# Optimization experiments

Measured on AMD Instinct MI355X. Metric: run time of the kernel, lower is better.

## Reference

```python
import jax, jax.numpy as jnp
import numpy as np
from jax import lax

LEAK = 0.2  # LeakyReLU negative slope used both in flow_conv and as act_type


def conv2d(x, w, b):
    # x: (N,Cin,H,W), w: (Cout,Cin,kh,kw) -> 'SAME' padding, stride 1
    out = lax.conv_general_dilated(x, w, (1, 1), 'SAME',
                                   dimension_numbers=('NCHW', 'OIHW', 'NCHW'))
    return out + b[None, :, None, None]


def leaky(x):
    return jnp.where(x >= 0, x, LEAK * x)


def bilinear_sample(im, ix, iy):
    # im: (C,H,W); ix,iy: (H,W) absolute pixel coords; zero padding (grid_sample default)
    C, H, W = im.shape
    x0 = jnp.floor(ix)
    y0 = jnp.floor(iy)

    def gather(xi, yi):
        valid = (xi >= 0) & (xi <= W - 1) & (yi >= 0) & (yi <= H - 1)
        xc = jnp.clip(xi, 0, W - 1).astype(jnp.int32)
        yc = jnp.clip(yi, 0, H - 1).astype(jnp.int32)
        return im[:, yc, xc] * valid[None].astype(im.dtype)

    wx1 = ix - x0
    wy1 = iy - y0
    wx0 = 1.0 - wx1
    wy0 = 1.0 - wy1
    return (gather(x0, y0) * (wx0 * wy0)[None]
            + gather(x0 + 1, y0) * (wx1 * wy0)[None]
            + gather(x0, y0 + 1) * (wx0 * wy1)[None]
            + gather(x0 + 1, y0 + 1) * (wx1 * wy1)[None])


def warp_all(h, flows):
    # h: (B,Ch,H,W); flows: (B,L,2,H,W). Matches warp(prev_h, -flow) with
    # torch F.grid_sample (bilinear, zero padding, align_corners=False).
    B, Ch, H, W = h.shape
    dt = h.dtype
    xx = jnp.arange(W, dtype=dt)
    yy = jnp.arange(H, dtype=dt)
    vx = xx[None, None, None, :] - flows[:, :, 0]  # grid + (-flow), x coord
    vy = yy[None, None, :, None] - flows[:, :, 1]
    xn = 2.0 * vx / max(W - 1, 1) - 1.0  # normalize to [-1,1]
    yn = 2.0 * vy / max(H - 1, 1) - 1.0
    ix = ((xn + 1.0) * W - 1.0) * 0.5  # unnormalize, align_corners=False
    iy = ((yn + 1.0) * H - 1.0) * 0.5
    samp = jax.vmap(jax.vmap(bilinear_sample, in_axes=(None, 0, 0)),
                    in_axes=(0, 0, 0))
    out = samp(h, ix, iy)  # (B,L,Ch,H,W)
    return out.reshape(B, -1, H, W)  # (B, L*Ch, H, W), same order as torch.cat


def setup_inputs() -> dict:
    key = jax.random.key(0)
    ks = jax.random.split(key, 8)
    B, S, C, H, W = 4, 6, 8, 96, 96
    Ch, L = 64, 13
    sc = lambda fan_in: 1.0 / np.sqrt(fan_in)
    return {
        'inputs': jax.random.normal(ks[0], (B, S, C, H, W), jnp.float32),
        'states': jnp.zeros((B, Ch, H, W), jnp.float32),
        'fw1': jax.random.normal(ks[1], (32, C + Ch, 3, 3), jnp.float32) * sc((C + Ch) * 9),
        'fb1': jnp.zeros((32,), jnp.float32),
        'fw2': jax.random.normal(ks[2], (2 * L, 32, 3, 3), jnp.float32) * sc(32 * 9),
        'fb2': jnp.zeros((2 * L,), jnp.float32),
        'i2h_w': jax.random.normal(ks[3], (3 * Ch, C, 3, 3), jnp.float32) * sc(C * 9),
        'i2h_b': jnp.zeros((3 * Ch,), jnp.float32),
        'ret_w': jax.random.normal(ks[4], (3 * Ch, L * Ch, 1, 1), jnp.float32) * sc(L * Ch),
        'ret_b': jnp.zeros((3 * Ch,), jnp.float32),
        'seq_len': 6,
    }


def reference(inputs, states, fw1, fb1, fw2, fb2, i2h_w, i2h_b, ret_w, ret_b, seq_len):
    B, S, C, H, W = inputs.shape
    Ch = states.shape[1]
    # precompute i2h over all timesteps (as in the torch module)
    i2h = conv2d(inputs.reshape(B * S, C, H, W), i2h_w, i2h_b)
    i2h = i2h.reshape(B, S, 3 * Ch, H, W)

    def step(h, xs):
        x_t, i2h_t = xs  # (B,C,H,W), (B,3Ch,H,W)
        f = leaky(conv2d(jnp.concatenate([x_t, h], axis=1), fw1, fb1))
        flows = conv2d(f, fw2, fb2)  # (B, 2L, H, W)
        flows = flows.reshape(B, flows.shape[1] // 2, 2, H, W)
        warped = warp_all(h, flows)  # (B, L*Ch, H, W)
        h2h = conv2d(warped, ret_w, ret_b)  # (B, 3Ch, H, W)
        i1, i2, i3 = jnp.split(i2h_t, 3, axis=1)
        h1, h2, h3 = jnp.split(h2h, 3, axis=1)
        r = jax.nn.sigmoid(i1 + h1)
        u = jax.nn.sigmoid(i2 + h2)
        m = leaky(i3 + r * h3)
        nh = u * h + (1.0 - u) * m
        return nh, nh

    xs = (jnp.moveaxis(inputs, 0, 1), jnp.moveaxis(i2h, 0, 1))  # time-major
    last_h, outs = lax.scan(step, states, xs)
    return jnp.moveaxis(outs, 0, 1), last_h  # ((B,S,Ch,H,W), (B,Ch,H,W))
```

## Files before the change

### kernel.cpp

```cpp
#include <hip/hip_runtime.h>
#include <hip/hip_bf16.h>
#include <math.h>

#define Bn 4
#define Sn 6
#define Cin 8
#define Hh 96
#define Ww 96
#define HW (Hh*Ww)
#define Chn 64
#define Ln 13
#define LCh (Ln*Chn)
#define OC3 (3*Chn)
#define LEAK 0.2f

typedef __hip_bfloat16 bf16;
typedef __attribute__((ext_vector_type(8))) short short8v;
typedef __attribute__((ext_vector_type(4))) short short4v;
typedef __attribute__((ext_vector_type(4))) float f32x4;

__device__ __forceinline__ float b2f(bf16 v){ return __bfloat162float(v); }
__device__ __forceinline__ bf16  f2b(float v){ return __float2bfloat16(v); }
__device__ __forceinline__ unsigned short bbits(bf16 v){ union{bf16 b; unsigned short s;} u; u.b=v; return u.s; }
__device__ __forceinline__ float us2f(unsigned short u){
    union{unsigned int i; float f;} x; x.i = ((unsigned)u)<<16; return x.f;
}
__device__ __forceinline__ const int4* rfl_ptr(const int4* p){
    uintptr_t v = (uintptr_t)p;
    int lo = __builtin_amdgcn_readfirstlane((int)(v & 0xFFFFFFFFu));
    int hi = __builtin_amdgcn_readfirstlane((int)(v >> 32));
    return (const int4*)(((uintptr_t)(unsigned)hi << 32) | (unsigned)lo);
}

__device__ __forceinline__ int4 mk_meta(float fx, float fy, int xc, int y){
    float ix = ((float)xc - fx) * (96.0f/95.0f) - 0.5f;
    float iy = ((float)y  - fy) * (96.0f/95.0f) - 0.5f;
    float x0f = floorf(ix), y0f = floorf(iy);
    float wx1 = ix - x0f,  wy1 = iy - y0f;
    float wx0 = 1.f - wx1, wy0 = 1.f - wy1;
    float vx0 = (x0f >=  0.f && x0f <= 95.f) ? 1.f : 0.f;
    float vx1 = (x0f >= -1.f && x0f <= 94.f) ? 1.f : 0.f;
    float vy0 = (y0f >=  0.f && y0f <= 95.f) ? 1.f : 0.f;
    float vy1 = (y0f >= -1.f && y0f <= 94.f) ? 1.f : 0.f;
    int xi0 = (int)fminf(fmaxf(x0f,      0.f), 95.f);
    int xi1 = (int)fminf(fmaxf(x0f+1.f,  0.f), 95.f);
    int yi0 = (int)fminf(fmaxf(y0f,      0.f), 95.f);
    int yi1 = (int)fminf(fmaxf(y0f+1.f,  0.f), 95.f);
    union { _Float16 h[2]; int i; } pz, pw;
    pz.h[0] = (_Float16)(wx0*wy0*vx0*vy0);
    pz.h[1] = (_Float16)(wx1*wy0*vx1*vy0);
    pw.h[0] = (_Float16)(wx0*wy1*vx0*vy1);
    pw.h[1] = (_Float16)(wx1*wy1*vx1*vy1);
    int4 m;
    m.x = (yi0*Ww+xi0) | ((yi0*Ww+xi1)<<16);
    m.y = (yi1*Ww+xi0) | ((yi1*Ww+xi1)<<16);
    m.z = pz.i; m.w = pw.i;
    return m;
}

__global__ void k_prep(const float* __restrict__ fw1, const float* __restrict__ fw2,
                       const float* __restrict__ wi,  const float* __restrict__ rw,
                       bf16* __restrict__ W1b, bf16* __restrict__ W2b,
                       bf16* __restrict__ Wi,  bf16* __restrict__ Wb)
{
    int i = blockIdx.x*256 + threadIdx.x;
    if (i < 21504){
        int oc = i/672, k = i%672; float v = 0.f;
        if (k < 648){ int tap = k/72, ic = k%72; v = fw1[(size_t)oc*648 + ic*9 + tap]; }
        W1b[i] = f2b(v);
    } else if (i < 30720){
        int j = i-21504; int oc = j/288, k = j%288; float v = 0.f;
        if (oc < 26){ int tap = k/32, ic = k%32; v = fw2[(size_t)oc*288 + ic*9 + tap]; }
        W2b[j] = f2b(v);
    } else if (i < 49152){
        int j = i-30720; int oc = j/96, k = j%96; float v = 0.f;
        if (k < 72){ int tap = k/8, ic = k%8; v = wi[(size_t)oc*72 + ic*9 + tap]; }
        Wi[j] = f2b(v);
    } else if (i < 208896){
        int j = i-49152; Wb[j] = f2b(rw[j]);
    }
}

__global__ void k_packx(const float* __restrict__ x, bf16* __restrict__ x_hwc)
{
    __shared__ unsigned short tx[8][68];
    int bs = blockIdx.y, pix0 = blockIdx.x*64, tid = threadIdx.x;
    #pragma unroll
    for (int it=0; it<2; ++it){
        int idx = it*256 + tid, ic = idx>>6, p = idx&63;
        tx[ic][p] = bbits(f2b(x[((size_t)bs*Cin + ic)*HW + pix0 + p]));
    }
    __syncthreads();
    unsigned short* dst = (unsigned short*)x_hwc;
    #pragma unroll
    for (int it=0; it<2; ++it){
        int j = it*256 + tid, p = j>>3, c = j&7;
        dst[((size_t)bs*HW + pix0 + p)*8 + c] = tx[c][p];
    }
}

__global__ void k_packh0(const float* __restrict__ s, bf16* __restrict__ hwc)
{
    __shared__ unsigned short t[64][65];
    int b = blockIdx.y, pix0 = blockIdx.x*64, tid = threadIdx.x;
    unsigned short* dst = (unsigned short*)hwc;
    #pragma unroll
    for (int it=0; it<16; ++it){
        int idx = it*256 + tid, c = idx>>6, p = idx&63;
        t[c][p] = bbits(f2b(s[((size_t)b*Chn + c)*HW + pix0 + p]));
    }
    __syncthreads();
    #pragma unroll
    for (int it=0; it<16; ++it){
        int idx = it*256 + tid, p = idx>>6, c = idx&63;
        dst[((size_t)b*HW + pix0 + p)*Chn + c] = t[c][p];
    }
}

__global__ __launch_bounds__(384) void k_front(const bf16* __restrict__ x_hwc,
        const bf16* __restrict__ h_hwc,
        const bf16* __restrict__ Wi,  const float* __restrict__ ib,
        const bf16* __restrict__ W1b, const float* __restrict__ fb1,
        bf16* __restrict__ i2h_hwc, bf16* __restrict__ f_hwc, int t)
{
    __shared__ bf16 tile[3*98*72];
    int y = blockIdx.x, b = blockIdx.y, tid = threadIdx.x;
    const bf16* xb = x_hwc + (size_t)(b*Sn + t)*HW*8;
    const bf16* hb = h_hwc + (size_t)b*HW*64;
    for (int s = tid; s < 294; s += 384){
        int r = s/98, px = s%98 - 1, yy = y + r - 1;
        float4* dst = (float4*)&tile[s*72];
        if (yy>=0 && yy<Hh && px>=0 && px<Ww){
            size_t gp = (size_t)yy*Ww + px;
            dst[0] = *(const float4*)(xb + gp*8);
            const float4* hsrc = (const float4*)(hb + gp*64);
            #pragma unroll
            for (int q=0;q<8;++q) dst[1+q] = hsrc[q];
        } else {
            float4 z{0,0,0,0};
            #pragma unroll
            for (int q=0;q<9;++q) dst[q] = z;
        }
    }
    __syncthreads();
    int wv = tid>>6, lane = tid&63, x0 = wv*16, n = lane&15, kg = lane>>4;
    int pix = y*Ww + x0 + n;

    {
        f32x4 acc[12];
        #pragma unroll
        for (int m=0;m<12;++m) acc[m] = f32x4{0,0,0,0};
        #pragma unroll
        for (int kk=0; kk<3; ++kk){
            int g = kk*4 + kg;
            int tap = (g > 8) ? 8 : g;
            int dy = tap/3, dx = tap%3;
            short8v bv = *(const short8v*)&tile[((dy*98) + (x0+n) + dx)*72];
            #pragma unroll
            for (int m=0;m<12;++m){
                short8v av = *(const short8v*)(Wi + (size_t)(m*16 + n)*96 + g*8);
                acc[m] = __builtin_amdgcn_mfma_f32_16x16x32_bf16(av, bv, acc[m], 0,0,0);
            }
        }
        size_t prow = ((size_t)b*HW + pix)*192;
        #pragma unroll
        for (int m=0;m<12;++m){
            short4v sv;
            #pragma unroll
            for (int r=0;r<4;++r){
                int oc = m*16 + kg*4 + r;
                sv[r] = (short)bbits(f2b(acc[m][r] + ib[oc]));
            }
            *(short4v*)&i2h_hwc[prow + m*16 + kg*4] = sv;
        }
    }

    {
        f32x4 acc0{0,0,0,0}, acc1{0,0,0,0};
        #pragma unroll
        for (int kk=0; kk<21; ++kk){
            int g = kk*4 + kg;
            int gc = (g > 80) ? 80 : g;
            int tap = gc/9, ch0 = (gc%9)*8;
            int dy = tap/3, dx = tap%3;
            short8v bv = *(const short8v*)&tile[(((dy*98) + (x0+n) + dx))*72 + ch0];
            short8v a0 = *(const short8v*)(W1b + (size_t)n*672 + g*8);
            short8v a1 = *(const short8v*)(W1b + (size_t)(16+n)*672 + g*8);
            acc0 = __builtin_amdgcn_mfma_f32_16x16x32_bf16(a0, bv, acc0, 0,0,0);
            acc1 = __builtin_amdgcn_mfma_f32_16x16x32_bf16(a1, bv, acc1, 0,0,0);
        }
        size_t prow = (size_t)b*HW + pix;
        #pragma unroll
        for (int mt=0; mt<2; ++mt){
            f32x4 a = mt ? acc1 : acc0;
            short4v sv;
            #pragma unroll
            for (int r=0;r<4;++r){
                int oc = mt*16 + kg*4 + r;
                float v = a[r] + fb1[oc];
                sv[r] = (short)bbits(f2b((v >= 0.f) ? v : LEAK*v));
            }
            *(short4v*)&f_hwc[prow*32 + mt*16 + kg*4] = sv;
        }
    }
}

__global__ __launch_bounds__(384) void k_conv2meta(const bf16* __restrict__ f_hwc,
        const bf16* __restrict__ W2b, const float* __restrict__ fb2,
        int4* __restrict__ meta)
{
    __shared__ bf16 tile[3*98*32];
    int y = blockIdx.x, b = blockIdx.y, tid = threadIdx.x;
    const bf16* fb = f_hwc + (size_t)b*HW*32;
    for (int s = tid; s < 294; s += 384){
        int r = s/98, px = s%98 - 1, yy = y + r - 1;
        float4* dst = (float4*)&tile[s*32];
        if (yy>=0 && yy<Hh && px>=0 && px<Ww){
            const float4* src = (const float4*)(fb + ((size_t)yy*Ww + px)*32);
            #pragma unroll
            for (int q=0;q<4;++q) dst[q] = src[q];
        } else {
            float4 z{0,0,0,0};
            #pragma unroll
            for (int q=0;q<4;++q) dst[q] = z;
        }
    }
    __syncthreads();
    int wv = tid>>6, lane = tid&63, x0 = wv*16, n = lane&15, kg = lane>>4;
    f32x4 acc0{0,0,0,0}, acc1{0,0,0,0};
    #pragma unroll
    for (int kk=0; kk<9; ++kk){
        int g = kk*4 + kg;
        int tap = g>>2, ch0 = (g&3)*8;
        int dy = tap/3, dx = tap%3;
        short8v bv = *(const short8v*)&tile[(((dy*98) + (x0+n) + dx))*32 + ch0];
        short8v a0 = *(const short8v*)(W2b + (size_t)n*288 + g*8);
        short8v a1 = *(const short8v*)(W2b + (size_t)(16+n)*288 + g*8);
        acc0 = __builtin_amdgcn_mfma_f32_16x16x32_bf16(a0, bv, acc0, 0,0,0);
        acc1 = __builtin_amdgcn_mfma_f32_16x16x32_bf16(a1, bv, acc1, 0,0,0);
    }
    int xc = x0 + n, pix = y*Ww + xc;
    int4* mb = meta + (size_t)b*Ln*HW + pix;
    {
        float v0 = acc0[0] + fb2[kg*4+0], v1 = acc0[1] + fb2[kg*4+1];
        float v2 = acc0[2] + fb2[kg*4+2], v3 = acc0[3] + fb2[kg*4+3];
        mb[(size_t)(2*kg  )*HW] = mk_meta(v0, v1, xc, y);
        mb[(size_t)(2*kg+1)*HW] = mk_meta(v2, v3, xc, y);
    }
    if (kg < 3){
        float v0 = acc1[0] + fb2[16+kg*4+0], v1 = acc1[1] + fb2[16+kg*4+1];
        mb[(size_t)(8+2*kg)*HW] = mk_meta(v0, v1, xc, y);
        if (kg < 2){
            float v2 = acc1[2] + fb2[16+kg*4+2], v3 = acc1[3] + fb2[16+kg*4+3];
            mb[(size_t)(9+2*kg)*HW] = mk_meta(v2, v3, xc, y);
        }
    }
}

__global__ __launch_bounds__(256) void k_fused(const int4* __restrict__ meta,
        const bf16* __restrict__ h_cur, const bf16* __restrict__ Wb,
        const float* __restrict__ rb, const bf16* __restrict__ i2h_hwc,
        bf16* __restrict__ h_nxt, float* __restrict__ out, int t)
{
    __shared__ bf16 wlds[32*LCh];
    char* ldsb = (char*)wlds;
    int tid = threadIdx.x, wv = tid>>6, lane = tid&63;
    int b = blockIdx.y, pix0 = blockIdx.x*32;
    const bf16* hb = h_cur + (size_t)b*HW*64;
    const unsigned short* hsu = (const unsigned short*)hb;
    int c = lane;

    const int4* mwp = rfl_ptr(meta + (size_t)b*Ln*HW + pix0 + wv);

    int mzA[8], mwA[8], mzB[8], mwB[8];
    unsigned short gA0[8], gA1[8], gA2[8], gA3[8];
    unsigned short gB0[8], gB1[8], gB2[8], gB3[8];

#define ISSUE(L, MZ, MW, G0, G1, G2, G3)                                \
    {                                                                   \
        _Pragma("unroll")                                               \
        for (int j=0;j<8;++j){                                          \
            int4 m = mwp[(size_t)(L)*HW + 4*j];                         \
            int sx = __builtin_amdgcn_readfirstlane(m.x);               \
            int sy = __builtin_amdgcn_readfirstlane(m.y);               \
            MZ[j] = __builtin_amdgcn_readfirstlane(m.z);                \
            MW[j] = __builtin_amdgcn_readfirstlane(m.w);                \
            G0[j] = hsu[(size_t)(sx & 0xFFFF)*64 + c];                  \
            G1[j] = hsu[(size_t)((unsigned)sx >> 16)*64 + c];           \
            G2[j] = hsu[(size_t)(sy & 0xFFFF)*64 + c];                  \
            G3[j] = hsu[(size_t)((unsigned)sy >> 16)*64 + c];           \
        }                                                               \
    }
#define CONSUME(L, MZ, MW, G0, G1, G2, G3)                              \
    {                                                                   \
        _Pragma("unroll")                                               \
        for (int j=0;j<8;++j){                                          \
            union { int i; _Float16 h[2]; } uz, uw;                     \
            uz.i = MZ[j]; uw.i = MW[j];                                 \
            float v = us2f(G0[j])*(float)uz.h[0]                        \
                    + us2f(G1[j])*(float)uz.h[1]                        \
                    + us2f(G2[j])*(float)uw.h[0]                        \
                    + us2f(G3[j])*(float)uw.h[1];                       \
            int px = wv + 4*j;                                          \
            *(bf16*)(ldsb + px*1664 + ((((L)*64 + c)*2) ^ ((px&7)<<4))) \
                = f2b(v);                                               \
        }                                                               \
    }

    ISSUE(0, mzA, mwA, gA0, gA1, gA2, gA3);
    ISSUE(1, mzB, mwB, gB0, gB1, gB2, gB3);
    CONSUME(0, mzA, mwA, gA0, gA1, gA2, gA3);
    ISSUE(2, mzA, mwA, gA0, gA1, gA2, gA3);
    CONSUME(1, mzB, mwB, gB0, gB1, gB2, gB3);
    ISSUE(3, mzB, mwB, gB0, gB1, gB2, gB3);
    CONSUME(2, mzA, mwA, gA0, gA1, gA2, gA3);
    ISSUE(4, mzA, mwA, gA0, gA1, gA2, gA3);
    CONSUME(3, mzB, mwB, gB0, gB1, gB2, gB3);
    ISSUE(5, mzB, mwB, gB0, gB1, gB2, gB3);
    CONSUME(4, mzA, mwA, gA0, gA1, gA2, gA3);
    ISSUE(6, mzA, mwA, gA0, gA1, gA2, gA3);
    CONSUME(5, mzB, mwB, gB0, gB1, gB2, gB3);
    ISSUE(7, mzB, mwB, gB0, gB1, gB2, gB3);
    CONSUME(6, mzA, mwA, gA0, gA1, gA2, gA3);
    ISSUE(8, mzA, mwA, gA0, gA1, gA2, gA3);
    CONSUME(7, mzB, mwB, gB0, gB1, gB2, gB3);
    ISSUE(9, mzB, mwB, gB0, gB1, gB2, gB3);
    CONSUME(8, mzA, mwA, gA0, gA1, gA2, gA3);
    ISSUE(10, mzA, mwA, gA0, gA1, gA2, gA3);
    CONSUME(9, mzB, mwB, gB0, gB1, gB2, gB3);
    ISSUE(11, mzB, mwB, gB0, gB1, gB2, gB3);
    CONSUME(10, mzA, mwA, gA0, gA1, gA2, gA3);
    ISSUE(12, mzA, mwA, gA0, gA1, gA2, gA3);
    CONSUME(11, mzB, mwB, gB0, gB1, gB2, gB3);
    CONSUME(12, mzA, mwA, gA0, gA1, gA2, gA3);
#undef ISSUE
#undef CONSUME

    int col = lane & 15, kg = lane >> 4;
    int pxa = pix0 + col, pxb = pxa + 16;
    short4v hva = *(const short4v*)&hb[(size_t)pxa*64 + wv*16 + kg*4];
    short4v hvb = *(const short4v*)&hb[(size_t)pxb*64 + wv*16 + kg*4];
    const bf16* ia = i2h_hwc + ((size_t)b*HW + pxa)*192 + wv*16 + kg*4;
    const bf16* ibp= i2h_hwc + ((size_t)b*HW + pxb)*192 + wv*16 + kg*4;
    short4v i1a = *(const short4v*)(ia);
    short4v i2a = *(const short4v*)(ia + 64);
    short4v i3a = *(const short4v*)(ia + 128);
    short4v i1b = *(const short4v*)(ibp);
    short4v i2b = *(const short4v*)(ibp + 64);
    short4v i3b = *(const short4v*)(ibp + 128);
    __syncthreads();

    const short8v* a0 = (const short8v*)(Wb + (size_t)((wv+0)*16+col)*LCh + kg*8);
    const short8v* a1 = (const short8v*)(Wb + (size_t)((wv+4)*16+col)*LCh + kg*8);
    const short8v* a2 = (const short8v*)(Wb + (size_t)((wv+8)*16+col)*LCh + kg*8);
    f32x4 c0a{0,0,0,0}, c1a{0,0,0,0}, c2a{0,0,0,0};
    f32x4 c0b{0,0,0,0}, c1b{0,0,0,0}, c2b{0,0,0,0};
    int swz = (col&7)<<4;
    #pragma unroll 2
    for (int kk=0; kk<26; ++kk){
        short8v av0 = a0[kk*4], av1 = a1[kk*4], av2 = a2[kk*4];
        int offa = col*1664 + ((kk*64 + kg*16) ^ swz);
        int offb = (col+16)*1664 + ((kk*64 + kg*16) ^ swz);
        short8v bva = *(const short8v*)(ldsb + offa);
        short8v bvb = *(const short8v*)(ldsb + offb);
        c0a = __builtin_amdgcn_mfma_f32_16x16x32_bf16(av0, bva, c0a, 0,0,0);
        c0b = __builtin_amdgcn_mfma_f32_16x16x32_bf16(av0, bvb, c0b, 0,0,0);
        c1a = __builtin_amdgcn_mfma_f32_16x16x32_bf16(av1, bva, c1a, 0,0,0);
        c1b = __builtin_amdgcn_mfma_f32_16x16x32_bf16(av1, bvb, c1b, 0,0,0);
        c2a = __builtin_amdgcn_mfma_f32_16x16x32_bf16(av2, bva, c2a, 0,0,0);
        c2b = __builtin_amdgcn_mfma_f32_16x16x32_bf16(av2, bvb, c2b, 0,0,0);
    }

    float nha[4], nhb[4];
    #pragma unroll
    for (int r=0; r<4; ++r){
        int cc = wv*16 + kg*4 + r;
        float h1 = c0a[r] + rb[cc];
        float h2 = c1a[r] + rb[cc+64];
        float h3 = c2a[r] + rb[cc+128];
        float rg = 1.f/(1.f + expf(-(us2f((unsigned short)i1a[r]) + h1)));
        float u  = 1.f/(1.f + expf(-(us2f((unsigned short)i2a[r]) + h2)));
        float mp = us2f((unsigned short)i3a[r]) + rg*h3;
        float m  = (mp >= 0.f) ? mp : LEAK*mp;
        float nh = u*us2f((unsigned short)hva[r]) + (1.f - u)*m;
        nha[r] = nh;
        out[(((size_t)(b*Sn+t))*Chn + cc)*HW + pxa] = nh;
        if (t == Sn-1)
            out[(size_t)Bn*Sn*Chn*HW + ((size_t)b*Chn + cc)*HW + pxa] = nh;
    }
    #pragma unroll
    for (int r=0; r<4; ++r){
        int cc = wv*16 + kg*4 + r;
        float h1 = c0b[r] + rb[cc];
        float h2 = c1b[r] + rb[cc+64];
        float h3 = c2b[r] + rb[cc+128];
        float rg = 1.f/(1.f + expf(-(us2f((unsigned short)i1b[r]) + h1)));
        float u  = 1.f/(1.f + expf(-(us2f((unsigned short)i2b[r]) + h2)));
        float mp = us2f((unsigned short)i3b[r]) + rg*h3;
        float m  = (mp >= 0.f) ? mp : LEAK*mp;
        float nh = u*us2f((unsigned short)hvb[r]) + (1.f - u)*m;
        nhb[r] = nh;
        out[(((size_t)(b*Sn+t))*Chn + cc)*HW + pxb] = nh;
        if (t == Sn-1)
            out[(size_t)Bn*Sn*Chn*HW + ((size_t)b*Chn + cc)*HW + pxb] = nh;
    }
    short4v sva, svb;
    #pragma unroll
    for (int r=0; r<4; ++r){
        sva[r] = (short)bbits(f2b(nha[r]));
        svb[r] = (short)bbits(f2b(nhb[r]));
    }
    *(short4v*)&h_nxt[((size_t)b*HW + pxa)*64 + wv*16 + kg*4] = sva;
    *(short4v*)&h_nxt[((size_t)b*HW + pxb)*64 + wv*16 + kg*4] = svb;
}

extern "C" void kernel_launch(void* const* d_in, const int* in_sizes, int n_in,
                              void* d_out, int out_size, void* d_ws, size_t ws_size,
                              hipStream_t stream) {
    const float* inputs = (const float*)d_in[0];
    const float* states = (const float*)d_in[1];
    const float* fw1    = (const float*)d_in[2];
    const float* fb1    = (const float*)d_in[3];
    const float* fw2    = (const float*)d_in[4];
    const float* fb2    = (const float*)d_in[5];
    const float* i2h_w  = (const float*)d_in[6];
    const float* i2h_b  = (const float*)d_in[7];
    const float* ret_w  = (const float*)d_in[8];
    const float* ret_b  = (const float*)d_in[9];
    float* out = (float*)d_out;

    char* ws = (char*)d_ws;
    bf16* h_hwcA  = (bf16*)(ws);
    bf16* h_hwcB  = (bf16*)(ws +  4718592);
    bf16* x_hwc   = (bf16*)(ws +  9437184);
    bf16* i2h_hwc = (bf16*)(ws + 12976128);
    bf16* f_hwc   = (bf16*)(ws + 27131904);
    int4* meta    = (int4*)(ws + 29491200);
    bf16* W1b     = (bf16*)(ws + 37158912);
    bf16* W2b     = (bf16*)(ws + 37201920);
    bf16* Wi      = (bf16*)(ws + 37220352);
    bf16* Wb      = (bf16*)(ws + 37257216);

    k_prep  <<<dim3(816),        256, 0, stream>>>(fw1, fw2, i2h_w, ret_w,
                                                   W1b, W2b, Wi, Wb);
    k_packx <<<dim3(144, Bn*Sn), 256, 0, stream>>>(inputs, x_hwc);
    k_packh0<<<dim3(144, Bn),    256, 0, stream>>>(states, h_hwcA);

    bf16* h_cur = h_hwcA;
    bf16* h_nxt = h_hwcB;
    for (int t = 0; t < Sn; ++t) {
        k_front    <<<dim3(96, Bn),  384, 0, stream>>>(x_hwc, h_cur, Wi, i2h_b,
                                                       W1b, fb1, i2h_hwc, f_hwc, t);
        k_conv2meta<<<dim3(96, Bn),  384, 0, stream>>>(f_hwc, W2b, fb2, meta);
        k_fused    <<<dim3(288, Bn), 256, 0, stream>>>(meta, h_cur, Wb, ret_b,
                                                       i2h_hwc, h_nxt, out, t);
        bf16* tmp = h_cur; h_cur = h_nxt; h_nxt = tmp;
    }
}
```

Measured before the change: 742.7 us.

## Double k_fused block to 512 threads, halving per-wave gather and MFMA work

k_fused now runs 8 waves per block instead of 4. Each wave gathers 4 pixels per flow instead of 8, and in the GEMM handles one 16-pixel half with three accumulators instead of two halves with six. This cuts per-thread registers and serial work so more waves can hide gather latency. In exchange, each Wb A-fragment is loaded by twice as many waves, and the 53KB LDS per block may limit how many blocks fit on a CU.

```diff
diff --git a/kernel.cpp b/kernel.cpp
--- a/kernel.cpp
+++ b/kernel.cpp
@@ -257,7 +257,7 @@
     }
 }
 
-__global__ __launch_bounds__(256) void k_fused(const int4* __restrict__ meta,
+__global__ __launch_bounds__(512, 4) void k_fused(const int4* __restrict__ meta,
         const bf16* __restrict__ h_cur, const bf16* __restrict__ Wb,
         const float* __restrict__ rb, const bf16* __restrict__ i2h_hwc,
         bf16* __restrict__ h_nxt, float* __restrict__ out, int t)
@@ -272,36 +272,36 @@
 
     const int4* mwp = rfl_ptr(meta + (size_t)b*Ln*HW + pix0 + wv);
 
-    int mzA[8], mwA[8], mzB[8], mwB[8];
-    unsigned short gA0[8], gA1[8], gA2[8], gA3[8];
-    unsigned short gB0[8], gB1[8], gB2[8], gB3[8];
+    int mzA[4], mwA[4], mzB[4], mwB[4];
+    unsigned short gA0[4], gA1[4], gA2[4], gA3[4];
+    unsigned short gB0[4], gB1[4], gB2[4], gB3[4];
 
 #define ISSUE(L, MZ, MW, G0, G1, G2, G3)                                \
     {                                                                   \
         _Pragma("unroll")                                               \
-        for (int j=0;j<8;++j){                                          \
-            int4 m = mwp[(size_t)(L)*HW + 4*j];                         \
+        for (int q=0;q<4;++q){                                          \
+            int4 m = mwp[(size_t)(L)*HW + 8*q];                         \
             int sx = __builtin_amdgcn_readfirstlane(m.x);               \
             int sy = __builtin_amdgcn_readfirstlane(m.y);               \
-            MZ[j] = __builtin_amdgcn_readfirstlane(m.z);                \
-            MW[j] = __builtin_amdgcn_readfirstlane(m.w);                \
-            G0[j] = hsu[(size_t)(sx & 0xFFFF)*64 + c];                  \
-            G1[j] = hsu[(size_t)((unsigned)sx >> 16)*64 + c];           \
-            G2[j] = hsu[(size_t)(sy & 0xFFFF)*64 + c];                  \
-            G3[j] = hsu[(size_t)((unsigned)sy >> 16)*64 + c];           \
+            MZ[q] = __builtin_amdgcn_readfirstlane(m.z);                \
+            MW[q] = __builtin_amdgcn_readfirstlane(m.w);                \
+            G0[q] = hsu[(size_t)(sx & 0xFFFF)*64 + c];                  \
+            G1[q] = hsu[(size_t)((unsigned)sx >> 16)*64 + c];           \
+            G2[q] = hsu[(size_t)(sy & 0xFFFF)*64 + c];                  \
+            G3[q] = hsu[(size_t)((unsigned)sy >> 16)*64 + c];           \
         }                                                               \
     }
 #define CONSUME(L, MZ, MW, G0, G1, G2, G3)                              \
     {                                                                   \
         _Pragma("unroll")                                               \
-        for (int j=0;j<8;++j){                                          \
+        for (int q=0;q<4;++q){                                          \
             union { int i; _Float16 h[2]; } uz, uw;                     \
-            uz.i = MZ[j]; uw.i = MW[j];                                 \
-            float v = us2f(G0[j])*(float)uz.h[0]                        \
-                    + us2f(G1[j])*(float)uz.h[1]                        \
-                    + us2f(G2[j])*(float)uw.h[0]                        \
-                    + us2f(G3[j])*(float)uw.h[1];                       \
-            int px = wv + 4*j;                                          \
+            uz.i = MZ[q]; uw.i = MW[q];                                 \
+            float v = us2f(G0[q])*(float)uz.h[0]                        \
+                    + us2f(G1[q])*(float)uz.h[1]                        \
+                    + us2f(G2[q])*(float)uw.h[0]                        \
+                    + us2f(G3[q])*(float)uw.h[1];                       \
+            int px = wv + 8*q;                                          \
             *(bf16*)(ldsb + px*1664 + ((((L)*64 + c)*2) ^ ((px&7)<<4))) \
                 = f2b(v);                                               \
         }                                                               \
@@ -337,44 +337,34 @@
 #undef CONSUME
 
     int col = lane & 15, kg = lane >> 4;
-    int pxa = pix0 + col, pxb = pxa + 16;
-    short4v hva = *(const short4v*)&hb[(size_t)pxa*64 + wv*16 + kg*4];
-    short4v hvb = *(const short4v*)&hb[(size_t)pxb*64 + wv*16 + kg*4];
-    const bf16* ia = i2h_hwc + ((size_t)b*HW + pxa)*192 + wv*16 + kg*4;
-    const bf16* ibp= i2h_hwc + ((size_t)b*HW + pxb)*192 + wv*16 + kg*4;
+    int half = wv & 1, mrow = wv >> 1;
+    int pxa = pix0 + half*16 + col;
+    short4v hva = *(const short4v*)&hb[(size_t)pxa*64 + mrow*16 + kg*4];
+    const bf16* ia = i2h_hwc + ((size_t)b*HW + pxa)*192 + mrow*16 + kg*4;
     short4v i1a = *(const short4v*)(ia);
     short4v i2a = *(const short4v*)(ia + 64);
     short4v i3a = *(const short4v*)(ia + 128);
-    short4v i1b = *(const short4v*)(ibp);
-    short4v i2b = *(const short4v*)(ibp + 64);
-    short4v i3b = *(const short4v*)(ibp + 128);
     __syncthreads();
 
-    const short8v* a0 = (const short8v*)(Wb + (size_t)((wv+0)*16+col)*LCh + kg*8);
-    const short8v* a1 = (const short8v*)(Wb + (size_t)((wv+4)*16+col)*LCh + kg*8);
-    const short8v* a2 = (const short8v*)(Wb + (size_t)((wv+8)*16+col)*LCh + kg*8);
+    const short8v* a0 = (const short8v*)(Wb + (size_t)((mrow+0)*16+col)*LCh + kg*8);
+    const short8v* a1 = (const short8v*)(Wb + (size_t)((mrow+4)*16+col)*LCh + kg*8);
+    const short8v* a2 = (const short8v*)(Wb + (size_t)((mrow+8)*16+col)*LCh + kg*8);
     f32x4 c0a{0,0,0,0}, c1a{0,0,0,0}, c2a{0,0,0,0};
-    f32x4 c0b{0,0,0,0}, c1b{0,0,0,0}, c2b{0,0,0,0};
+    int pcol = half*16 + col;
     int swz = (col&7)<<4;
     #pragma unroll 2
     for (int kk=0; kk<26; ++kk){
         short8v av0 = a0[kk*4], av1 = a1[kk*4], av2 = a2[kk*4];
-        int offa = col*1664 + ((kk*64 + kg*16) ^ swz);
-        int offb = (col+16)*1664 + ((kk*64 + kg*16) ^ swz);
-        short8v bva = *(const short8v*)(ldsb + offa);
-        short8v bvb = *(const short8v*)(ldsb + offb);
+        short8v bva = *(const short8v*)(ldsb + pcol*1664 + ((kk*64 + kg*16) ^ swz));
         c0a = __builtin_amdgcn_mfma_f32_16x16x32_bf16(av0, bva, c0a, 0,0,0);
-        c0b = __builtin_amdgcn_mfma_f32_16x16x32_bf16(av0, bvb, c0b, 0,0,0);
         c1a = __builtin_amdgcn_mfma_f32_16x16x32_bf16(av1, bva, c1a, 0,0,0);
-        c1b = __builtin_amdgcn_mfma_f32_16x16x32_bf16(av1, bvb, c1b, 0,0,0);
         c2a = __builtin_amdgcn_mfma_f32_16x16x32_bf16(av2, bva, c2a, 0,0,0);
-        c2b = __builtin_amdgcn_mfma_f32_16x16x32_bf16(av2, bvb, c2b, 0,0,0);
-    }
-
-    float nha[4], nhb[4];
+    }
+
+    float nha[4];
     #pragma unroll
     for (int r=0; r<4; ++r){
-        int cc = wv*16 + kg*4 + r;
+        int cc = mrow*16 + kg*4 + r;
         float h1 = c0a[r] + rb[cc];
         float h2 = c1a[r] + rb[cc+64];
         float h3 = c2a[r] + rb[cc+128];
@@ -388,30 +378,10 @@
         if (t == Sn-1)
             out[(size_t)Bn*Sn*Chn*HW + ((size_t)b*Chn + cc)*HW + pxa] = nh;
     }
-    #pragma unroll
-    for (int r=0; r<4; ++r){
-        int cc = wv*16 + kg*4 + r;
-        float h1 = c0b[r] + rb[cc];
-        float h2 = c1b[r] + rb[cc+64];
-        float h3 = c2b[r] + rb[cc+128];
-        float rg = 1.f/(1.f + expf(-(us2f((unsigned short)i1b[r]) + h1)));
-        float u  = 1.f/(1.f + expf(-(us2f((unsigned short)i2b[r]) + h2)));
-        float mp = us2f((unsigned short)i3b[r]) + rg*h3;
-        float m  = (mp >= 0.f) ? mp : LEAK*mp;
-        float nh = u*us2f((unsigned short)hvb[r]) + (1.f - u)*m;
-        nhb[r] = nh;
-        out[(((size_t)(b*Sn+t))*Chn + cc)*HW + pxb] = nh;
-        if (t == Sn-1)
-            out[(size_t)Bn*Sn*Chn*HW + ((size_t)b*Chn + cc)*HW + pxb] = nh;
-    }
-    short4v sva, svb;
-    #pragma unroll
-    for (int r=0; r<4; ++r){
-        sva[r] = (short)bbits(f2b(nha[r]));
-        svb[r] = (short)bbits(f2b(nhb[r]));
-    }
-    *(short4v*)&h_nxt[((size_t)b*HW + pxa)*64 + wv*16 + kg*4] = sva;
-    *(short4v*)&h_nxt[((size_t)b*HW + pxb)*64 + wv*16 + kg*4] = svb;
+    short4v sva;
+    #pragma unroll
+    for (int r=0; r<4; ++r) sva[r] = (short)bbits(f2b(nha[r]));
+    *(short4v*)&h_nxt[((size_t)b*HW + pxa)*64 + mrow*16 + kg*4] = sva;
 }
 
 extern "C" void kernel_launch(void* const* d_in, const int* in_sizes, int n_in,
@@ -452,7 +422,7 @@
         k_front    <<<dim3(96, Bn),  384, 0, stream>>>(x_hwc, h_cur, Wi, i2h_b,
                                                        W1b, fb1, i2h_hwc, f_hwc, t);
         k_conv2meta<<<dim3(96, Bn),  384, 0, stream>>>(f_hwc, W2b, fb2, meta);
-        k_fused    <<<dim3(288, Bn), 256, 0, stream>>>(meta, h_cur, Wb, ret_b,
+        k_fused    <<<dim3(288, Bn), 512, 0, stream>>>(meta, h_cur, Wb, ret_b,
                                                        i2h_hwc, h_nxt, out, t);
         bf16* tmp = h_cur; h_cur = h_nxt; h_nxt = tmp;
     }
```

Result: slower. 960.6 us (+29.3%).
